# Performance work log

Measured on AMD Instinct MI355X. Metric: run time of the kernel, lower is better.

## Reference

```python
import jax, jax.numpy as jnp
import numpy as np

T = 128        # number of timesteps (init arg T)
LEN_M = 32     # causal window length (init arg len_M)
N = 8192       # nodes
F = 64         # features per node


def setup_inputs() -> dict:
    key = jax.random.key(0)
    k1, k2, k3 = jax.random.split(key, 3)
    X = jax.random.normal(k1, (T, N, F), dtype=jnp.float32)
    # M_pad[r] holds the length-(r+1) parameter M[str(r+1)] in its first r+1 slots
    # (padding is masked out before softmax, so its values are irrelevant).
    M_pad = jax.random.normal(k2, (LEN_M, LEN_M), dtype=jnp.float32)
    # M_big[j] corresponds to parameter key str(LEN_M+1+j); keys LEN_M+1..T-1 are
    # used by rows LEN_M+1..T-1 (row LEN_M reuses M[str(LEN_M)] = M_pad[-1], per the source).
    M_big = jax.random.normal(k3, (T - LEN_M - 1, LEN_M), dtype=jnp.float32)
    return {"X": X, "M_pad": M_pad, "M_big": M_big}


def _band_weights(M_pad, M_big):
    """Build the [T, T] causal banded mixing matrix with per-row softmax weights."""
    cols = jnp.arange(LEN_M)
    # rows 0..LEN_M-1: softmax over the growing prefix window of length row+1
    prefix_mask = cols[None, :] <= jnp.arange(LEN_M)[:, None]            # [LEN_M, LEN_M]
    w_small = jax.nn.softmax(jnp.where(prefix_mask, M_pad, -jnp.inf), axis=1)
    # rows LEN_M..T-1 use key str(row): row==LEN_M reuses M_pad[-1], rest use M_big
    logits_big = jnp.concatenate([M_pad[LEN_M - 1:LEN_M], M_big], axis=0)  # [T-LEN_M, LEN_M]
    w_big = jax.nn.softmax(logits_big, axis=1)
    W = jnp.zeros((T, T), dtype=M_pad.dtype)
    W = W.at[:LEN_M, :LEN_M].set(w_small)  # w_small is zero outside the prefix window
    rows = jnp.arange(LEN_M, T)
    cidx = (rows - LEN_M + 1)[:, None] + cols[None, :]  # sliding window cols per row
    W = W.at[rows[:, None], cidx].set(w_big)
    return W


def reference(X, M_pad, M_big):
    W = _band_weights(M_pad, M_big)          # [T, T] banded
    data = X.reshape(T, -1)                  # [T, N*F]
    out = W @ data                           # causal windowed weighted sum, all rows at once
    return out.reshape(X.shape)
```

## Files before the change

kernel.cpp:

```cpp
#include <hip/hip_runtime.h>
#include <math.h>

#define T_    128
#define LENM  32
#define NCOL  (8192 * 64)

typedef float f2 __attribute__((ext_vector_type(2)));

__global__ void build_w_kernel(const float* __restrict__ M_pad,
                               const float* __restrict__ M_big,
                               float* __restrict__ Wc) {
    int t = threadIdx.x;
    if (t >= T_) return;
    const float* src;
    int len, joff;
    if (t < LENM)       { src = M_pad + t * LENM;              len = t + 1; joff = LENM - 1 - t; }
    else if (t == LENM) { src = M_pad + (LENM - 1) * LENM;     len = LENM;  joff = 0; }
    else                { src = M_big + (t - LENM - 1) * LENM; len = LENM;  joff = 0; }

    float m = -3.4e38f;
    for (int j = 0; j < len; ++j) m = fmaxf(m, src[j]);
    float e[LENM];
    float s = 0.f;
    for (int j = 0; j < len; ++j) { e[j] = expf(src[j] - m); s += e[j]; }
    float inv = 1.f / s;
    for (int j = 0; j < LENM; ++j) Wc[t * LENM + j] = 0.f;
    for (int j = 0; j < len; ++j)  Wc[t * LENM + joff + j] = e[j] * inv;
}

__global__ __launch_bounds__(256) void band_mix_kernel(
    const float* __restrict__ X,
    const float* __restrict__ Wc,
    float* __restrict__ out) {
    __shared__ float4 w4[T_ * LENM / 4];
    for (int i = threadIdx.x; i < T_ * LENM / 4; i += 256)
        w4[i] = reinterpret_cast<const float4*>(Wc)[i];
    __syncthreads();

    const int c = (blockIdx.x * 256 + threadIdx.x) * 2;
    const f2* xp = reinterpret_cast<const f2*>(X + c);
    f2* op = reinterpret_cast<f2*>(out + c);
    const size_t rs = NCOL / 2;

    f2 a[LENM], b[LENM];
#pragma unroll
    for (int i = 0; i < LENM; ++i) { a[i].x = 0.f; a[i].y = 0.f; }

#define DO_CHUNK(K, CUR, PRV)                                                 \
    {                                                                         \
        _Pragma("unroll")                                                     \
        for (int i = 0; i < LENM; ++i)                                        \
            CUR[i] = xp[(size_t)((K) * LENM + i) * rs];                       \
        _Pragma("unroll")                                                     \
        for (int i = 0; i < LENM; ++i) {                                      \
            const int row = (K) * LENM + i;                                   \
            f2 acc; acc.x = 0.f; acc.y = 0.f;                                 \
            _Pragma("unroll")                                                 \
            for (int q = 0; q < 8; ++q) {                                     \
                float4 w = w4[row * 8 + q];                                   \
                _Pragma("unroll")                                             \
                for (int m = 0; m < 4; ++m) {                                 \
                    const int j = q * 4 + m;                                  \
                    float wm = (m == 0) ? w.x : (m == 1) ? w.y                \
                             : (m == 2) ? w.z : w.w;                          \
                    f2 xv = (j < LENM - 1 - i) ? PRV[i + 1 + j]               \
                                               : CUR[i + j - (LENM - 1)];     \
                    acc.x = fmaf(wm, xv.x, acc.x);                            \
                    acc.y = fmaf(wm, xv.y, acc.y);                            \
                }                                                             \
            }                                                                 \
            __builtin_nontemporal_store(acc, &op[(size_t)row * rs]);          \
        }                                                                     \
    }

    DO_CHUNK(0, b, a)
    DO_CHUNK(1, a, b)
    DO_CHUNK(2, b, a)
    DO_CHUNK(3, a, b)
#undef DO_CHUNK
}

extern "C" void kernel_launch(void* const* d_in, const int* in_sizes, int n_in,
                              void* d_out, int out_size, void* d_ws, size_t ws_size,
                              hipStream_t stream) {
    const float* X     = (const float*)d_in[0];
    const float* M_pad = (const float*)d_in[1];
    const float* M_big = (const float*)d_in[2];
    float* out = (float*)d_out;
    float* Wc  = (float*)d_ws;

    build_w_kernel<<<1, 128, 0, stream>>>(M_pad, M_big, Wc);
    band_mix_kernel<<<NCOL / 2 / 256, 256, 0, stream>>>(X, Wc, out);
}
```

Measured before the change: 101.4 us.

## Widen columns per thread to four and stream loads eight rows ahead

Each thread now handles four columns with 128-bit loads and stores instead of two, which halves the grid. Row loads are issued as a rolling prefetch eight rows ahead of the current output row, replacing the old batch of 32 loads per chunk. The structurally zero weights in the first 32 rows are skipped at compile time, and launch bounds ask for two blocks per CU. The cost is register pressure from two 32-entry float4 arrays, which risks spills or low occupancy, and the halved grid leaves fewer waves to hide memory latency.

```diff
diff --git a/kernel.cpp b/kernel.cpp
--- a/kernel.cpp
+++ b/kernel.cpp
@@ -5,7 +5,7 @@
 #define LENM  32
 #define NCOL  (8192 * 64)
 
-typedef float f2 __attribute__((ext_vector_type(2)));
+typedef float f4_t __attribute__((ext_vector_type(4)));
 
 __global__ void build_w_kernel(const float* __restrict__ M_pad,
                                const float* __restrict__ M_big,
@@ -28,56 +28,78 @@
     for (int j = 0; j < len; ++j)  Wc[t * LENM + joff + j] = e[j] * inv;
 }
 
-__global__ __launch_bounds__(256) void band_mix_kernel(
+template<int R>
+__device__ __forceinline__ void step(const f4_t* __restrict__ xp,
+                                     f4_t* __restrict__ op,
+                                     const f4_t* w4,
+                                     f4_t (&A)[LENM], f4_t (&B)[LENM]) {
+    constexpr int K     = R / LENM;
+    constexpr int i_    = R % LENM;
+    constexpr int jmin_ = (R < LENM) ? (LENM - 1 - i_) : 0;
+    f4_t (&CUR)[LENM] = (K & 1) ? B : A;
+    f4_t (&PRV)[LENM] = (K & 1) ? A : B;
+    const size_t rs = NCOL / 4;
+
+    if constexpr (R + 8 < T_) {
+        f4_t ld = xp[(size_t)(R + 8) * rs];
+        if constexpr (i_ < LENM - 8) CUR[i_ + 8] = ld;
+        else                         PRV[i_ - (LENM - 8)] = ld;
+    }
+
+    f4_t acc; acc.x = 0.f; acc.y = 0.f; acc.z = 0.f; acc.w = 0.f;
+#pragma unroll
+    for (int q = 0; q < 8; ++q) {
+        if (q * 4 + 3 >= jmin_) {
+            f4_t w = w4[R * 8 + q];
+#pragma unroll
+            for (int m = 0; m < 4; ++m) {
+                const int j = q * 4 + m;
+                if (j >= jmin_) {
+                    f4_t xv = (j < LENM - 1 - i_) ? PRV[i_ + 1 + j]
+                                                  : CUR[i_ + j - (LENM - 1)];
+                    float wm = (m == 0) ? w.x : (m == 1) ? w.y
+                             : (m == 2) ? w.z : w.w;
+                    acc.x = fmaf(wm, xv.x, acc.x);
+                    acc.y = fmaf(wm, xv.y, acc.y);
+                    acc.z = fmaf(wm, xv.z, acc.z);
+                    acc.w = fmaf(wm, xv.w, acc.w);
+                }
+            }
+        }
+    }
+    __builtin_nontemporal_store(acc, &op[(size_t)R * rs]);
+}
+
+template<int R>
+__device__ __forceinline__ void run_steps(const f4_t* __restrict__ xp,
+                                          f4_t* __restrict__ op,
+                                          const f4_t* w4,
+                                          f4_t (&A)[LENM], f4_t (&B)[LENM]) {
+    if constexpr (R < T_) {
+        step<R>(xp, op, w4, A, B);
+        run_steps<R + 1>(xp, op, w4, A, B);
+    }
+}
+
+__global__ __launch_bounds__(256, 2) void band_mix_kernel(
     const float* __restrict__ X,
     const float* __restrict__ Wc,
     float* __restrict__ out) {
-    __shared__ float4 w4[T_ * LENM / 4];
+    __shared__ f4_t w4[T_ * LENM / 4];
     for (int i = threadIdx.x; i < T_ * LENM / 4; i += 256)
-        w4[i] = reinterpret_cast<const float4*>(Wc)[i];
+        w4[i] = reinterpret_cast<const f4_t*>(Wc)[i];
     __syncthreads();
 
-    const int c = (blockIdx.x * 256 + threadIdx.x) * 2;
-    const f2* xp = reinterpret_cast<const f2*>(X + c);
-    f2* op = reinterpret_cast<f2*>(out + c);
-    const size_t rs = NCOL / 2;
+    const int c = (blockIdx.x * 256 + threadIdx.x) * 4;
+    const f4_t* xp = reinterpret_cast<const f4_t*>(X + c);
+    f4_t* op = reinterpret_cast<f4_t*>(out + c);
+    const size_t rs = NCOL / 4;
 
-    f2 a[LENM], b[LENM];
+    f4_t A[LENM], B[LENM];
 #pragma unroll
-    for (int i = 0; i < LENM; ++i) { a[i].x = 0.f; a[i].y = 0.f; }
+    for (int i = 0; i < 8; ++i) A[i] = xp[(size_t)i * rs];
 
-#define DO_CHUNK(K, CUR, PRV)                                                 \
-    {                                                                         \
-        _Pragma("unroll")                                                     \
-        for (int i = 0; i < LENM; ++i)                                        \
-            CUR[i] = xp[(size_t)((K) * LENM + i) * rs];                       \
-        _Pragma("unroll")                                                     \
-        for (int i = 0; i < LENM; ++i) {                                      \
-            const int row = (K) * LENM + i;                                   \
-            f2 acc; acc.x = 0.f; acc.y = 0.f;                                 \
-            _Pragma("unroll")                                                 \
-            for (int q = 0; q < 8; ++q) {                                     \
-                float4 w = w4[row * 8 + q];                                   \
-                _Pragma("unroll")                                             \
-                for (int m = 0; m < 4; ++m) {                                 \
-                    const int j = q * 4 + m;                                  \
-                    float wm = (m == 0) ? w.x : (m == 1) ? w.y                \
-                             : (m == 2) ? w.z : w.w;                          \
-                    f2 xv = (j < LENM - 1 - i) ? PRV[i + 1 + j]               \
-                                               : CUR[i + j - (LENM - 1)];     \
-                    acc.x = fmaf(wm, xv.x, acc.x);                            \
-                    acc.y = fmaf(wm, xv.y, acc.y);                            \
-                }                                                             \
-            }                                                                 \
-            __builtin_nontemporal_store(acc, &op[(size_t)row * rs]);          \
-        }                                                                     \
-    }
-
-    DO_CHUNK(0, b, a)
-    DO_CHUNK(1, a, b)
-    DO_CHUNK(2, b, a)
-    DO_CHUNK(3, a, b)
-#undef DO_CHUNK
+    run_steps<0>(xp, op, w4, A, B);
 }
 
 extern "C" void kernel_launch(void* const* d_in, const int* in_sizes, int n_in,
@@ -90,5 +112,5 @@
     float* Wc  = (float*)d_ws;
 
     build_w_kernel<<<1, 128, 0, stream>>>(M_pad, M_big, Wc);
-    band_mix_kernel<<<NCOL / 2 / 256, 256, 0, stream>>>(X, Wc, out);
+    band_mix_kernel<<<NCOL / 4 / 256, 256, 0, stream>>>(X, Wc, out);
 }
```

Result: faster. 95.32 us (-6.0%).
